# Optimization experiments

Measured on AMD Instinct MI355X. Metric: run time of the kernel, lower is better.

## Reference

```python
import jax, jax.numpy as jnp
import numpy as np

N = 8192
D = 256
DENSITY = 0.02  # ~164 neighbors per node


def setup_inputs() -> dict:
    key = jax.random.key(0)
    k1, k2, k3, k4 = jax.random.split(key, 4)
    inputs = jax.random.normal(k1, (N, D), dtype=jnp.float32)
    vals = jax.random.uniform(k2, (N, N), dtype=jnp.float32, minval=0.1, maxval=1.0)
    mask = jax.random.uniform(k3, (N, N), dtype=jnp.float32) < DENSITY
    adj = jnp.where(mask, vals, 0.0)
    H_v = 0.1 * jax.random.normal(k4, (D, 1), dtype=jnp.float32)
    return {"inputs": inputs, "adj": adj, "H_v": H_v}


def reference(inputs, adj, H_v):
    # scores[j] = inputs[j] . H_v  -> sparse values v_ij = adj_ij * scores[j]
    scores = jnp.squeeze(inputs @ H_v, -1)            # [N]
    mask = adj != 0.0                                  # nonzero pattern of SparseTensor
    logits = adj * scores[None, :]                     # [N, N]
    neg = jnp.asarray(jnp.finfo(logits.dtype).min, logits.dtype)
    logits = jnp.where(mask, logits, neg)
    # sparse softmax: normalize only over nonzero entries per row
    m = jnp.max(logits, axis=1, keepdims=True)
    e = jnp.where(mask, jnp.exp(logits - m), 0.0)
    s = jnp.sum(e, axis=1, keepdims=True)
    weights = e / jnp.where(s > 0, s, 1.0)             # empty rows -> all-zero weights
    # sparse_tensor_dense_matmul(weights, inputs)
    return weights @ inputs                            # [N, D]
```

## Files before the change

kernel.cpp:

```cpp
#include <hip/hip_runtime.h>

#define NN 8192
#define DD 256
#define CHUNK 1024

__global__ __launch_bounds__(256) void scores_kernel(const float* __restrict__ inputs,
                                                     const float* __restrict__ Hv,
                                                     float* __restrict__ scores) {
    int wave = threadIdx.x >> 6;
    int lane = threadIdx.x & 63;
    int row  = blockIdx.x * 4 + wave;
    if (row >= NN) return;
    float4 v = ((const float4*)(inputs + (size_t)row * DD))[lane];
    float4 h = ((const float4*)Hv)[lane];
    float s = v.x * h.x + v.y * h.y + v.z * h.z + v.w * h.w;
    #pragma unroll
    for (int off = 32; off > 0; off >>= 1) s += __shfl_down(s, off, 64);
    if (lane == 0) scores[row] = s;
}

__global__ __launch_bounds__(256) void attn_kernel(const float* __restrict__ adj,
                                                   const float* __restrict__ inputs,
                                                   const float* __restrict__ scores,
                                                   float* __restrict__ out) {
    __shared__ int   s_j[CHUNK];
    __shared__ float s_e[CHUNK];
    __shared__ int   s_cnt;

    const int row = blockIdx.x;
    const int tid = threadIdx.x;
    const float* __restrict__ arow = adj + (size_t)row * NN;

    float acc  = 0.0f;
    float ssum = 0.0f;

    for (int base = 0; base < NN; base += CHUNK) {
        if (tid == 0) s_cnt = 0;
        __syncthreads();

        float4 a = ((const float4*)(arow + base))[tid];
        int j0 = base + tid * 4;
        if (a.x != 0.0f) { int k = atomicAdd(&s_cnt, 1); s_j[k] = j0 + 0; s_e[k] = __expf(a.x * scores[j0 + 0]); }
        if (a.y != 0.0f) { int k = atomicAdd(&s_cnt, 1); s_j[k] = j0 + 1; s_e[k] = __expf(a.y * scores[j0 + 1]); }
        if (a.z != 0.0f) { int k = atomicAdd(&s_cnt, 1); s_j[k] = j0 + 2; s_e[k] = __expf(a.z * scores[j0 + 2]); }
        if (a.w != 0.0f) { int k = atomicAdd(&s_cnt, 1); s_j[k] = j0 + 3; s_e[k] = __expf(a.w * scores[j0 + 3]); }
        __syncthreads();

        const int cnt = s_cnt;
        for (int k = 0; k < cnt; ++k) {
            float e = s_e[k];
            int   j = s_j[k];
            acc  += e * inputs[(size_t)j * DD + tid];
            ssum += e;
        }
        __syncthreads();
    }

    float r = (ssum > 0.0f) ? (acc / ssum) : 0.0f;
    out[(size_t)row * DD + tid] = r;
}

extern "C" void kernel_launch(void* const* d_in, const int* in_sizes, int n_in,
                              void* d_out, int out_size, void* d_ws, size_t ws_size,
                              hipStream_t stream) {
    const float* inputs = (const float*)d_in[0];
    const float* adj    = (const float*)d_in[1];
    const float* Hv     = (const float*)d_in[2];
    float* out = (float*)d_out;
    float* scores = (float*)d_ws;

    scores_kernel<<<NN / 4, 256, 0, stream>>>(inputs, Hv, scores);
    attn_kernel<<<NN, 256, 0, stream>>>(adj, inputs, scores, out);
}
```

Baseline: 471.1 us.

## Compact full adjacency row via prefix scan and split gather across waves

New measurement: 432.8 us. 1.09x faster.

```diff
diff --git a/kernel.cpp b/kernel.cpp
--- a/kernel.cpp
+++ b/kernel.cpp
@@ -2,7 +2,7 @@
 
 #define NN 8192
 #define DD 256
-#define CHUNK 1024
+#define CAP 2048
 
 __global__ __launch_bounds__(256) void scores_kernel(const float* __restrict__ inputs,
                                                      const float* __restrict__ Hv,
@@ -19,45 +19,114 @@
     if (lane == 0) scores[row] = s;
 }
 
+__device__ __forceinline__ void gather_accum(const float2* s_je, int total,
+                                             const float* __restrict__ inputs,
+                                             int lane4, int wave,
+                                             float4& acc, float& ssum) {
+    int k = wave;
+    for (; k + 12 < total; k += 16) {
+        float2 je0 = s_je[k];
+        float2 je1 = s_je[k + 4];
+        float2 je2 = s_je[k + 8];
+        float2 je3 = s_je[k + 12];
+        const float4 v0 = *(const float4*)(inputs + (size_t)__float_as_int(je0.x) * DD + lane4);
+        const float4 v1 = *(const float4*)(inputs + (size_t)__float_as_int(je1.x) * DD + lane4);
+        const float4 v2 = *(const float4*)(inputs + (size_t)__float_as_int(je2.x) * DD + lane4);
+        const float4 v3 = *(const float4*)(inputs + (size_t)__float_as_int(je3.x) * DD + lane4);
+        acc.x += je0.y * v0.x; acc.y += je0.y * v0.y; acc.z += je0.y * v0.z; acc.w += je0.y * v0.w;
+        acc.x += je1.y * v1.x; acc.y += je1.y * v1.y; acc.z += je1.y * v1.z; acc.w += je1.y * v1.w;
+        acc.x += je2.y * v2.x; acc.y += je2.y * v2.y; acc.z += je2.y * v2.z; acc.w += je2.y * v2.w;
+        acc.x += je3.y * v3.x; acc.y += je3.y * v3.y; acc.z += je3.y * v3.z; acc.w += je3.y * v3.w;
+        ssum += je0.y + je1.y + je2.y + je3.y;
+    }
+    for (; k < total; k += 4) {
+        float2 je = s_je[k];
+        const float4 v = *(const float4*)(inputs + (size_t)__float_as_int(je.x) * DD + lane4);
+        acc.x += je.y * v.x; acc.y += je.y * v.y; acc.z += je.y * v.z; acc.w += je.y * v.w;
+        ssum += je.y;
+    }
+}
+
 __global__ __launch_bounds__(256) void attn_kernel(const float* __restrict__ adj,
                                                    const float* __restrict__ inputs,
                                                    const float* __restrict__ scores,
                                                    float* __restrict__ out) {
-    __shared__ int   s_j[CHUNK];
-    __shared__ float s_e[CHUNK];
+    __shared__ float2 s_je[CAP];
+    __shared__ int   s_wsum[4];
+    __shared__ float s_ssum[4];
     __shared__ int   s_cnt;
+    __shared__ float s_red[4 * DD];
 
-    const int row = blockIdx.x;
-    const int tid = threadIdx.x;
-    const float* __restrict__ arow = adj + (size_t)row * NN;
+    const int row   = blockIdx.x;
+    const int tid   = threadIdx.x;
+    const int lane  = tid & 63;
+    const int wave  = tid >> 6;
+    const int lane4 = lane * 4;
 
-    float acc  = 0.0f;
-    float ssum = 0.0f;
+    const float4* arow4 = (const float4*)(adj + (size_t)row * NN);
+    float4 a[8];
+#pragma unroll
+    for (int c = 0; c < 8; ++c) a[c] = arow4[c * 256 + tid];
 
-    for (int base = 0; base < NN; base += CHUNK) {
-        if (tid == 0) s_cnt = 0;
-        __syncthreads();
+    int nz = 0;
+#pragma unroll
+    for (int c = 0; c < 8; ++c)
+        nz += (a[c].x != 0.f) + (a[c].y != 0.f) + (a[c].z != 0.f) + (a[c].w != 0.f);
 
-        float4 a = ((const float4*)(arow + base))[tid];
-        int j0 = base + tid * 4;
-        if (a.x != 0.0f) { int k = atomicAdd(&s_cnt, 1); s_j[k] = j0 + 0; s_e[k] = __expf(a.x * scores[j0 + 0]); }
-        if (a.y != 0.0f) { int k = atomicAdd(&s_cnt, 1); s_j[k] = j0 + 1; s_e[k] = __expf(a.y * scores[j0 + 1]); }
-        if (a.z != 0.0f) { int k = atomicAdd(&s_cnt, 1); s_j[k] = j0 + 2; s_e[k] = __expf(a.z * scores[j0 + 2]); }
-        if (a.w != 0.0f) { int k = atomicAdd(&s_cnt, 1); s_j[k] = j0 + 3; s_e[k] = __expf(a.w * scores[j0 + 3]); }
-        __syncthreads();
+    int pre = nz;
+#pragma unroll
+    for (int off = 1; off < 64; off <<= 1) {
+        int t = __shfl_up(pre, off, 64);
+        if (lane >= off) pre += t;
+    }
+    if (lane == 63) s_wsum[wave] = pre;
+    __syncthreads();
+    int base = 0, total = 0;
+#pragma unroll
+    for (int w = 0; w < 4; ++w) {
+        int t = s_wsum[w];
+        if (w < wave) base += t;
+        total += t;
+    }
 
-        const int cnt = s_cnt;
-        for (int k = 0; k < cnt; ++k) {
-            float e = s_e[k];
-            int   j = s_j[k];
-            acc  += e * inputs[(size_t)j * DD + tid];
-            ssum += e;
+    float4 acc = make_float4(0.f, 0.f, 0.f, 0.f);
+    float ssum = 0.f;
+
+    if (total <= CAP) {
+        int off = base + pre - nz;
+#pragma unroll
+        for (int c = 0; c < 8; ++c) {
+            int j0 = c * 1024 + tid * 4;
+            float v;
+            v = a[c].x; if (v != 0.f) { s_je[off++] = make_float2(__int_as_float(j0 + 0), __expf(v * scores[j0 + 0])); }
+            v = a[c].y; if (v != 0.f) { s_je[off++] = make_float2(__int_as_float(j0 + 1), __expf(v * scores[j0 + 1])); }
+            v = a[c].z; if (v != 0.f) { s_je[off++] = make_float2(__int_as_float(j0 + 2), __expf(v * scores[j0 + 2])); }
+            v = a[c].w; if (v != 0.f) { s_je[off++] = make_float2(__int_as_float(j0 + 3), __expf(v * scores[j0 + 3])); }
         }
         __syncthreads();
+        gather_accum(s_je, total, inputs, lane4, wave, acc, ssum);
+    } else {
+        for (int c = 0; c < 8; ++c) {
+            if (tid == 0) s_cnt = 0;
+            __syncthreads();
+            int j0 = c * 1024 + tid * 4;
+            float v;
+            v = a[c].x; if (v != 0.f) { int k = atomicAdd(&s_cnt, 1); s_je[k] = make_float2(__int_as_float(j0 + 0), __expf(v * scores[j0 + 0])); }
+            v = a[c].y; if (v != 0.f) { int k = atomicAdd(&s_cnt, 1); s_je[k] = make_float2(__int_as_float(j0 + 1), __expf(v * scores[j0 + 1])); }
+            v = a[c].z; if (v != 0.f) { int k = atomicAdd(&s_cnt, 1); s_je[k] = make_float2(__int_as_float(j0 + 2), __expf(v * scores[j0 + 2])); }
+            v = a[c].w; if (v != 0.f) { int k = atomicAdd(&s_cnt, 1); s_je[k] = make_float2(__int_as_float(j0 + 3), __expf(v * scores[j0 + 3])); }
+            __syncthreads();
+            gather_accum(s_je, s_cnt, inputs, lane4, wave, acc, ssum);
+            __syncthreads();
+        }
     }
 
-    float r = (ssum > 0.0f) ? (acc / ssum) : 0.0f;
-    out[(size_t)row * DD + tid] = r;
+    if (lane == 0) s_ssum[wave] = ssum;
+    *(float4*)&s_red[wave * DD + lane4] = acc;
+    __syncthreads();
+    float tot = s_ssum[0] + s_ssum[1] + s_ssum[2] + s_ssum[3];
+    float r = s_red[0 * DD + tid] + s_red[1 * DD + tid] + s_red[2 * DD + tid] + s_red[3 * DD + tid];
+    out[(size_t)row * DD + tid] = (tot > 0.f) ? r / tot : 0.f;
 }
 
 extern "C" void kernel_launch(void* const* d_in, const int* in_sizes, int n_in,
```

## Replace gather-based sparse attention with dense bf16 MFMA matmul over adjacency

Applied to the files above, without the earlier changes.

New measurement: 464.2 us. About the same (-1.5%).

```diff
diff --git a/kernel.cpp b/kernel.cpp
--- a/kernel.cpp
+++ b/kernel.cpp
@@ -2,7 +2,24 @@
 
 #define NN 8192
 #define DD 256
-#define CHUNK 1024
+#define RT 32
+#define KC 128
+#define NCHUNK (NN / KC)
+
+typedef float v4f __attribute__((ext_vector_type(4)));
+typedef short short8 __attribute__((ext_vector_type(8)));
+typedef float f32x4 __attribute__((ext_vector_type(4)));
+typedef unsigned short u16x4 __attribute__((ext_vector_type(4)));
+typedef unsigned short u16x8 __attribute__((ext_vector_type(8)));
+
+__device__ __forceinline__ unsigned short f2bf_rne(float x) {
+    unsigned u = __float_as_uint(x);
+    u += 0x7fffu + ((u >> 16) & 1u);
+    return (unsigned short)(u >> 16);
+}
+__device__ __forceinline__ float bf_to_f(unsigned short b) {
+    return __uint_as_float((unsigned)b << 16);
+}
 
 __global__ __launch_bounds__(256) void scores_kernel(const float* __restrict__ inputs,
                                                      const float* __restrict__ Hv,
@@ -19,45 +36,157 @@
     if (lane == 0) scores[row] = s;
 }
 
-__global__ __launch_bounds__(256) void attn_kernel(const float* __restrict__ adj,
-                                                   const float* __restrict__ inputs,
-                                                   const float* __restrict__ scores,
-                                                   float* __restrict__ out) {
-    __shared__ int   s_j[CHUNK];
-    __shared__ float s_e[CHUNK];
+#define XP 258
+__global__ __launch_bounds__(256) void xt_kernel(const float* __restrict__ inputs,
+                                                 unsigned short* __restrict__ xt) {
+    __shared__ unsigned short sx[64 * XP];
+    const int tid = threadIdx.x;
+    const int k0  = blockIdx.x * 64;
+    #pragma unroll
+    for (int r = 0; r < 16; ++r) {
+        int row = r * 4 + (tid >> 6);
+        int col = (tid & 63) * 4;
+        float4 v = *(const float4*)(inputs + (size_t)(k0 + row) * DD + col);
+        u16x4 w;
+        w[0] = f2bf_rne(v.x); w[1] = f2bf_rne(v.y); w[2] = f2bf_rne(v.z); w[3] = f2bf_rne(v.w);
+        *(u16x4*)&sx[row * XP + col] = w;
+    }
+    __syncthreads();
+    #pragma unroll
+    for (int rep = 0; rep < 8; ++rep) {
+        int n  = rep * 32 + (tid >> 3);
+        int kg = (tid & 7) * 8;
+        u16x8 w;
+        #pragma unroll
+        for (int j = 0; j < 8; ++j) w[j] = sx[(kg + j) * XP + n];
+        *(u16x8*)(xt + (size_t)n * NN + k0 + kg) = w;
+    }
+}
+
+__global__ __launch_bounds__(512, 1) void spmm_kernel(const float* __restrict__ adj,
+                                                      const unsigned short* __restrict__ xt,
+                                                      const float* __restrict__ scores,
+                                                      float* __restrict__ out) {
+    __shared__ unsigned short sE[2][RT * KC];
+    __shared__ float s_den[RT];
+
+    const int tid  = threadIdx.x;
+    const int lane = tid & 63;
+    const int wave = tid >> 6;
+    const int q    = lane >> 4;
+    const int m16  = lane & 15;
+    const int row0 = blockIdx.x * RT;
+
+    const int lrow = tid >> 4;
+    const int kgb  = tid & 15;
+    const int kg   = kgb * 8;
+    const float* arow = adj + (size_t)(row0 + lrow) * NN;
+
+    f32x4 acc[2][2] = {};
+    float den = 0.f;
+
+    v4f a0 = __builtin_nontemporal_load((const v4f*)(arow + kg));
+    v4f a1 = __builtin_nontemporal_load((const v4f*)(arow + kg + 4));
+    float4 s0 = *(const float4*)(scores + kg);
+    float4 s1 = *(const float4*)(scores + kg + 4);
+
+    for (int c = 0; c < NCHUNK; ++c) {
+        const int cn = (c + 1 < NCHUNK ? c + 1 : c) * KC;
+        v4f na0 = __builtin_nontemporal_load((const v4f*)(arow + cn + kg));
+        v4f na1 = __builtin_nontemporal_load((const v4f*)(arow + cn + kg + 4));
+        float4 ns0 = *(const float4*)(scores + cn + kg);
+        float4 ns1 = *(const float4*)(scores + cn + kg + 4);
+
+        float af[8] = { a0.x, a0.y, a0.z, a0.w, a1.x, a1.y, a1.z, a1.w };
+        float sf[8] = { s0.x, s0.y, s0.z, s0.w, s1.x, s1.y, s1.z, s1.w };
+        u16x8 ev;
+        #pragma unroll
+        for (int i = 0; i < 8; ++i) {
+            float e = (af[i] != 0.f) ? __expf(af[i] * sf[i]) : 0.f;
+            unsigned short b = f2bf_rne(e);
+            ev[i] = b;
+            den += bf_to_f(b);
+        }
+        *(u16x8*)&sE[c & 1][lrow * KC + ((kgb ^ (lrow & 15)) * 8)] = ev;
+        __syncthreads();
+
+        const unsigned short* Eb = sE[c & 1];
+        short8 afr[2][4];
+        #pragma unroll
+        for (int mt = 0; mt < 2; ++mt)
+            #pragma unroll
+            for (int kh = 0; kh < 4; ++kh) {
+                int m = mt * 16 + m16;
+                afr[mt][kh] = *(const short8*)&Eb[m * KC + (((kh * 4 + q) ^ m16) * 8)];
+            }
+        short8 bfr[2][4];
+        #pragma unroll
+        for (int nt = 0; nt < 2; ++nt)
+            #pragma unroll
+            for (int kh = 0; kh < 4; ++kh) {
+                int n = wave * 32 + nt * 16 + m16;
+                bfr[nt][kh] = *(const short8*)(xt + (size_t)n * NN + c * KC + kh * 32 + q * 8);
+            }
+        #pragma unroll
+        for (int mt = 0; mt < 2; ++mt)
+            #pragma unroll
+            for (int nt = 0; nt < 2; ++nt)
+                #pragma unroll
+                for (int kh = 0; kh < 4; ++kh)
+                    acc[mt][nt] = __builtin_amdgcn_mfma_f32_16x16x32_bf16(
+                        afr[mt][kh], bfr[nt][kh], acc[mt][nt], 0, 0, 0);
+
+        a0 = na0; a1 = na1; s0 = ns0; s1 = ns1;
+    }
+
+    #pragma unroll
+    for (int d = 1; d < 16; d <<= 1) den += __shfl_xor(den, d, 64);
+    if ((tid & 15) == 0) s_den[lrow] = den;
+    __syncthreads();
+
+    #pragma unroll
+    for (int mt = 0; mt < 2; ++mt)
+        #pragma unroll
+        for (int nt = 0; nt < 2; ++nt)
+            #pragma unroll
+            for (int r = 0; r < 4; ++r) {
+                int rr = mt * 16 + q * 4 + r;
+                float dn = s_den[rr];
+                float v = (dn > 0.f) ? acc[mt][nt][r] / dn : 0.f;
+                out[(size_t)(row0 + rr) * DD + wave * 32 + nt * 16 + m16] = v;
+            }
+}
+
+__global__ __launch_bounds__(256) void attn_fallback(const float* __restrict__ adj,
+                                                     const float* __restrict__ inputs,
+                                                     const float* __restrict__ scores,
+                                                     float* __restrict__ out) {
+    __shared__ int   s_j[1024];
+    __shared__ float s_e[1024];
     __shared__ int   s_cnt;
-
     const int row = blockIdx.x;
     const int tid = threadIdx.x;
-    const float* __restrict__ arow = adj + (size_t)row * NN;
-
-    float acc  = 0.0f;
-    float ssum = 0.0f;
-
-    for (int base = 0; base < NN; base += CHUNK) {
+    const float* arow = adj + (size_t)row * NN;
+    float acc = 0.f, ssum = 0.f;
+    for (int base = 0; base < NN; base += 1024) {
         if (tid == 0) s_cnt = 0;
         __syncthreads();
-
         float4 a = ((const float4*)(arow + base))[tid];
         int j0 = base + tid * 4;
-        if (a.x != 0.0f) { int k = atomicAdd(&s_cnt, 1); s_j[k] = j0 + 0; s_e[k] = __expf(a.x * scores[j0 + 0]); }
-        if (a.y != 0.0f) { int k = atomicAdd(&s_cnt, 1); s_j[k] = j0 + 1; s_e[k] = __expf(a.y * scores[j0 + 1]); }
-        if (a.z != 0.0f) { int k = atomicAdd(&s_cnt, 1); s_j[k] = j0 + 2; s_e[k] = __expf(a.z * scores[j0 + 2]); }
-        if (a.w != 0.0f) { int k = atomicAdd(&s_cnt, 1); s_j[k] = j0 + 3; s_e[k] = __expf(a.w * scores[j0 + 3]); }
-        __syncthreads();
-
-        const int cnt = s_cnt;
-        for (int k = 0; k < cnt; ++k) {
+        if (a.x != 0.f) { int k = atomicAdd(&s_cnt, 1); s_j[k] = j0 + 0; s_e[k] = __expf(a.x * scores[j0 + 0]); }
+        if (a.y != 0.f) { int k = atomicAdd(&s_cnt, 1); s_j[k] = j0 + 1; s_e[k] = __expf(a.y * scores[j0 + 1]); }
+        if (a.z != 0.f) { int k = atomicAdd(&s_cnt, 1); s_j[k] = j0 + 2; s_e[k] = __expf(a.z * scores[j0 + 2]); }
+        if (a.w != 0.f) { int k = atomicAdd(&s_cnt, 1); s_j[k] = j0 + 3; s_e[k] = __expf(a.w * scores[j0 + 3]); }
+        __syncthreads();
+        int c = s_cnt;
+        for (int k = 0; k < c; ++k) {
             float e = s_e[k];
-            int   j = s_j[k];
-            acc  += e * inputs[(size_t)j * DD + tid];
+            acc  += e * inputs[(size_t)s_j[k] * DD + tid];
             ssum += e;
         }
         __syncthreads();
     }
-
-    float r = (ssum > 0.0f) ? (acc / ssum) : 0.0f;
-    out[(size_t)row * DD + tid] = r;
+    out[(size_t)row * DD + tid] = (ssum > 0.f) ? acc / ssum : 0.f;
 }
 
 extern "C" void kernel_launch(void* const* d_in, const int* in_sizes, int n_in,
@@ -67,8 +196,18 @@
     const float* adj    = (const float*)d_in[1];
     const float* Hv     = (const float*)d_in[2];
     float* out = (float*)d_out;
-    float* scores = (float*)d_ws;
+
+    char* ws = (char*)d_ws;
+    float*          scores = (float*)ws;
+    unsigned short* xt     = (unsigned short*)(ws + 32768);
+
+    const size_t need = 32768 + (size_t)DD * NN * sizeof(unsigned short);
 
     scores_kernel<<<NN / 4, 256, 0, stream>>>(inputs, Hv, scores);
-    attn_kernel<<<NN, 256, 0, stream>>>(adj, inputs, scores, out);
-}
+    if (ws_size >= need) {
+        xt_kernel<<<NN / 64, 256, 0, stream>>>(inputs, xt);
+        spmm_kernel<<<NN / RT, 512, 0, stream>>>(adj, xt, scores, out);
+    } else {
+        attn_fallback<<<NN, 256, 0, stream>>>(adj, inputs, scores, out);
+    }
+}
```
